# Kernel tuning notes

Hardware: AMD Instinct MI355X
Metric: run time of the kernel (lower is better)

The kernel has to match this reference:

```python
import jax, jax.numpy as jnp
import numpy as np

NUM_HEADS = 4
GROUPS = 8
EPS = 1e-5


def setup_inputs() -> dict:
    key = jax.random.key(0)
    ks = jax.random.split(key, 8)
    B, C, H, W = 8, 512, 64, 64
    L, E = 77, 768
    std = 0.02
    return {
        "x": jax.random.normal(ks[0], (B, C, H, W), jnp.float32),
        "text_emb": jax.random.normal(ks[1], (B, L, E), jnp.float32),
        "attention_mask": jax.random.randint(ks[2], (B, L), 0, 2, jnp.int32),
        "Wq_w": jax.random.normal(ks[3], (C, C), jnp.float32) * std,
        "Wq_b": jnp.zeros((C,), jnp.float32),
        "Wk_w": jax.random.normal(ks[4], (C, E), jnp.float32) * std,
        "Wk_b": jnp.zeros((C,), jnp.float32),
        "Wv_w": jax.random.normal(ks[5], (C, E), jnp.float32) * std,
        "Wv_b": jnp.zeros((C,), jnp.float32),
        "gn_scale": jnp.ones((C,), jnp.float32),
        "gn_bias": jnp.zeros((C,), jnp.float32),
    }


def reference(x, text_emb, attention_mask, Wq_w, Wq_b, Wk_w, Wk_b, Wv_w, Wv_b, gn_scale, gn_bias):
    B, C, H, W = x.shape
    dh = C // NUM_HEADS
    scale = dh ** -0.5

    # [B, HW, C] queries from image features
    x_flat = x.reshape(B, C, H * W).transpose(0, 2, 1)
    Q = x_flat @ Wq_w.T + Wq_b                 # [B, S, C]
    K = text_emb @ Wk_w.T + Wk_b               # [B, L, C]
    V = text_emb @ Wv_w.T + Wv_b               # [B, L, C]

    def split_heads(t):
        Bt, T, _ = t.shape
        return t.reshape(Bt, T, NUM_HEADS, dh).transpose(0, 2, 1, 3)  # [B, h, T, dh]

    Qh, Kh, Vh = split_heads(Q), split_heads(K), split_heads(V)

    scores = jnp.einsum("bhqd,bhkd->bhqk", Qh, Kh) * scale  # [B, h, S, L]
    mask = (attention_mask == 0)[:, None, None, :]
    scores = jnp.where(mask, -jnp.inf, scores)
    probs = jax.nn.softmax(scores, axis=-1)
    # dropout layers are identity in eval mode
    attn = jnp.einsum("bhqk,bhkd->bhqd", probs, Vh)          # [B, h, S, dh]

    out = attn.transpose(0, 2, 1, 3).reshape(B, H * W, C)    # [B, S, C]
    out = out.transpose(0, 2, 1).reshape(B, C, H, W)

    # GroupNorm(8 groups, affine) over (C/G, H, W) per group
    g = out.reshape(B, GROUPS, -1)
    mean = g.mean(axis=-1, keepdims=True)
    var = g.var(axis=-1, keepdims=True)
    g = (g - mean) * jax.lax.rsqrt(var + EPS)
    out = g.reshape(B, C, H, W) * gn_scale[None, :, None, None] + gn_bias[None, :, None, None]
    return out
```

## Files before the change

kernel.cpp:

```cpp
#include <hip/hip_runtime.h>
#include <hip/hip_bf16.h>
#include <cstdint>


typedef __attribute__((ext_vector_type(8))) short short8;
typedef __attribute__((ext_vector_type(4))) short short4v;
typedef __attribute__((ext_vector_type(4))) float f32x4;

#define DEV __device__ __forceinline__

DEV float bf2f(unsigned short u){ union{uint32_t i; float f;} x; x.i = ((uint32_t)u) << 16; return x.f; }
DEV unsigned short f2bf(float f){ __hip_bfloat16 h = __float2bfloat16(&f ? f : f); return *reinterpret_cast<unsigned short*>(&h); }
DEV short8 ld8(const unsigned short* p){ return *reinterpret_cast<const short8*>(p); }
DEV f32x4 ldf4(const float* p){ return *reinterpret_cast<const f32x4*>(p); }

#if defined(__has_builtin)
#if __has_builtin(__builtin_amdgcn_global_load_lds)
#define HAVE_ASYNC_LDS 1
#endif
#endif

__global__ __launch_bounds__(256) void k_fat(const float* __restrict__ x,
                                             unsigned short* __restrict__ xT,
                                             const float* __restrict__ text,
                                             const float* __restrict__ Wk,
                                             const float* __restrict__ Wkb,
                                             const float* __restrict__ Wv,
                                             const float* __restrict__ Wvb,
                                             unsigned short* __restrict__ wsK,
                                             unsigned short* __restrict__ wsVt,
                                             const float* __restrict__ Wq,
                                             unsigned short* __restrict__ wsWqT,
                                             int b0, int s_base, int slen, int SB){
  __shared__ unsigned short U[10368];
  const int tid = threadIdx.x;
  const int bx = blockIdx.x, by = blockIdx.y, bz = blockIdx.z;
  const int bg = b0 + bz;

  if (bx < 64){
    if (bx * 64 >= slen) return;
    unsigned short* t = U;
    const int s0 = s_base + bx * 64, c0 = by * 64;
    #pragma unroll
    for (int it = 0; it < 2; ++it){
      int slot = tid + it * 256;
      int r = slot >> 3, sg = slot & 7;
      int sw = sg ^ (r >> 3);
      const float* src = &x[((size_t)(bg * 512 + c0 + r)) * 4096 + s0 + sg * 8];
      f32x4 a = ldf4(src), b = ldf4(src + 4);
      short8 v;
      #pragma unroll
      for (int j = 0; j < 4; ++j){ v[j] = (short)f2bf(a[j]); v[j + 4] = (short)f2bf(b[j]); }
      *reinterpret_cast<short8*>(&t[r * 72 + sw * 8]) = v;
    }
    __syncthreads();
    #pragma unroll
    for (int it = 0; it < 2; ++it){
      int slot = tid + it * 256;
      int j = slot >> 3, i8 = slot & 7;
      short8 v;
      #pragma unroll
      for (int q = 0; q < 8; ++q){
        int c = i8 * 8 + q;
        int sw = (j >> 3) ^ i8;
        v[q] = (short)t[c * 72 + sw * 8 + (j & 7)];
      }
      *reinterpret_cast<short8*>(&xT[((size_t)(bz * slen) + bx * 64 + j) * 512 + c0 + i8 * 8]) = v;
    }
  } else if (bx < 66){
    unsigned short* At = U;
    unsigned short* Bt = U + 5760;
    const int wave = tid >> 6, lane = tid & 63;
    const int m16 = lane & 15, quad = lane >> 4;
    const int uc = (bx - 64) * 8 + by;
    const int u0 = uc * 64;
    const bool isK = (u0 < 512);
    const float* W  = isK ? Wk  : Wv;
    const float* Wb = isK ? Wkb : Wvb;
    const int c0 = u0 & 511;
    const int c  = c0 + wave * 16 + m16;
    f32x4 acc[5];
    #pragma unroll
    for (int mt = 0; mt < 5; ++mt) acc[mt] = (f32x4){0.f, 0.f, 0.f, 0.f};
    for (int kc = 0; kc < 12; ++kc){
      const int e0 = kc * 64;
      #pragma unroll
      for (int it = 0; it < 9; ++it){
        int slot = tid + it * 256;
        if (slot < 1280){
          int row = slot >> 4, e4 = (slot & 15) * 4;
          f32x4 v = (row < 77) ? ldf4(&text[((size_t)(bg * 77 + row)) * 768 + e0 + e4])
                               : (f32x4){0.f, 0.f, 0.f, 0.f};
          short4v o;
          #pragma unroll
          for (int j = 0; j < 4; ++j) o[j] = (short)f2bf(v[j]);
          *reinterpret_cast<short4v*>(&At[row * 72 + e4]) = o;
        } else {
          int bs = slot - 1280;
          int row = bs >> 4, e4 = (bs & 15) * 4;
          f32x4 v = ldf4(&W[((size_t)(c0 + row)) * 768 + e0 + e4]);
          short4v o;
          #pragma unroll
          for (int j = 0; j < 4; ++j) o[j] = (short)f2bf(v[j]);
          *reinterpret_cast<short4v*>(&Bt[row * 72 + e4]) = o;
        }
      }
      __syncthreads();
      #pragma unroll
      for (int kk = 0; kk < 64; kk += 32){
        short8 bf_ = *reinterpret_cast<const short8*>(&Bt[(wave * 16 + m16) * 72 + kk + quad * 8]);
        #pragma unroll
        for (int mt = 0; mt < 5; ++mt){
          short8 af_ = *reinterpret_cast<const short8*>(&At[(mt * 16 + m16) * 72 + kk + quad * 8]);
          acc[mt] = __builtin_amdgcn_mfma_f32_16x16x32_bf16(af_, bf_, acc[mt], 0, 0, 0);
        }
      }
      __syncthreads();
    }
    const float bias = Wb[c];
    if (isK){
      #pragma unroll
      for (int mt = 0; mt < 5; ++mt)
        #pragma unroll
        for (int r = 0; r < 4; ++r){
          int l = mt * 16 + quad * 4 + r;
          if (l < 77) wsK[((size_t)(bz * 77 + l)) * 512 + c] = f2bf(acc[mt][r] + bias);
        }
    } else {
      unsigned short* vr = &wsVt[((size_t)(bz * 512 + c)) * 96];
      #pragma unroll
      for (int mt = 0; mt < 5; ++mt){
        short4v pk;
        #pragma unroll
        for (int r = 0; r < 4; ++r) pk[r] = (short)f2bf(acc[mt][r] + bias);
        *reinterpret_cast<short4v*>(&vr[mt * 16 + quad * 4]) = pk;
      }
      short4v z = {};
      *reinterpret_cast<short4v*>(&vr[80 + quad * 4]) = z;
    }
  } else {
    unsigned short* t = U;
    const int nb = 8 * SB;
    const int p  = by + bz * 8;
    for (int tile = p; tile < 64; tile += nb){
      const int ti = tile >> 3, tj = tile & 7;
      #pragma unroll
      for (int it = 0; it < 2; ++it){
        int slot = tid + it * 256;
        int r = slot >> 3, sg = slot & 7;
        int sw = sg ^ (r >> 3);
        const float* src = &Wq[((size_t)(tj * 64 + r)) * 512 + ti * 64 + sg * 8];
        f32x4 a = ldf4(src), b2 = ldf4(src + 4);
        short8 v;
        #pragma unroll
        for (int j = 0; j < 4; ++j){ v[j] = (short)f2bf(a[j]); v[j + 4] = (short)f2bf(b2[j]); }
        *reinterpret_cast<short8*>(&t[r * 72 + sw * 8]) = v;
      }
      __syncthreads();
      #pragma unroll
      for (int it = 0; it < 2; ++it){
        int slot = tid + it * 256;
        int j = slot >> 3, i8 = slot & 7;
        short8 v;
        #pragma unroll
        for (int q = 0; q < 8; ++q){
          int dd = i8 * 8 + q;
          int sw = (j >> 3) ^ i8;
          v[q] = (short)t[dd * 72 + sw * 8 + (j & 7)];
        }
        *reinterpret_cast<short8*>(&wsWqT[((size_t)(ti * 64 + j)) * 512 + tj * 64 + i8 * 8]) = v;
      }
      __syncthreads();
    }
  }
}

__global__ __launch_bounds__(256) void k1b(const unsigned short* __restrict__ wsWqT,
                                           const unsigned short* __restrict__ wsK,
                                           const float* __restrict__ Wqb,
                                           unsigned short* __restrict__ wsKWq,
                                           float* __restrict__ kbias){
  const int tid = threadIdx.x;
  const int wave = tid >> 6, lane = tid & 63;
  const int m16 = lane & 15, quad = lane >> 4;
  const int cq = blockIdx.x, h = blockIdx.y, bz = blockIdx.z;
  const int cbase = cq * 128 + wave * 32;

  f32x4 acc[2][5];
  #pragma unroll
  for (int mt = 0; mt < 2; ++mt)
    #pragma unroll
    for (int nt = 0; nt < 5; ++nt) acc[mt][nt] = (f32x4){0.f, 0.f, 0.f, 0.f};

  #pragma unroll
  for (int ks = 0; ks < 4; ++ks){
    short8 aw[2];
    #pragma unroll
    for (int mt = 0; mt < 2; ++mt)
      aw[mt] = ld8(&wsWqT[(size_t)(cbase + mt * 16 + m16) * 512 + h * 128 + ks * 32 + quad * 8]);
    #pragma unroll
    for (int nt = 0; nt < 5; ++nt){
      int l = nt * 16 + m16;
      short8 bk = {};
      if (l < 77) bk = ld8(&wsK[((size_t)(bz * 77 + l)) * 512 + h * 128 + ks * 32 + quad * 8]);
      #pragma unroll
      for (int mt = 0; mt < 2; ++mt)
        acc[mt][nt] = __builtin_amdgcn_mfma_f32_16x16x32_bf16(aw[mt], bk, acc[mt][nt], 0, 0, 0);
    }
  }
  #pragma unroll
  for (int mt = 0; mt < 2; ++mt)
    #pragma unroll
    for (int nt = 0; nt < 5; ++nt){
      int l = nt * 16 + m16;
      short4v pk;
      #pragma unroll
      for (int r = 0; r < 4; ++r) pk[r] = (short)f2bf(acc[mt][nt][r]);
      *reinterpret_cast<short4v*>(&wsKWq[((size_t)((bz * 4 + h) * 80 + l)) * 512 + cbase + mt * 16 + quad * 4]) = pk;
    }
  if (cq == 0 && tid < 80){
    int l = tid;
    float kb = 0.f;
    if (l < 77){
      #pragma unroll
      for (int d = 0; d < 128; d += 8){
        short8 kv = ld8(&wsK[((size_t)(bz * 77 + l)) * 512 + h * 128 + d]);
        f32x4 wa = ldf4(&Wqb[h * 128 + d]);
        f32x4 wb = ldf4(&Wqb[h * 128 + d + 4]);
        #pragma unroll
        for (int j = 0; j < 4; ++j){
          kb += bf2f((unsigned short)kv[j]) * wa[j];
          kb += bf2f((unsigned short)kv[j + 4]) * wb[j];
        }
      }
    }
    kbias[(bz * 4 + h) * 80 + l] = kb;
  }
}

__global__ __launch_bounds__(256, 4) void k2_attn(const unsigned short* __restrict__ xT,
                                                  const unsigned short* __restrict__ wsKWq,
                                                  const unsigned short* __restrict__ wsVt,
                                                  const int* __restrict__ amask,
                                                  const float* __restrict__ kbias,
                                                  float* __restrict__ out,
                                                  float* __restrict__ gnacc,
                                                  int b0, int s_base, int slen){
  __shared__ unsigned short arena[13312];
  __shared__ float maskf[96];
  unsigned short* Pt = arena;

  const int tid = threadIdx.x;
  const int wave = tid >> 6, lane = tid & 63;
  const int m16 = lane & 15, quad = lane >> 4;
  const int st = blockIdx.x, h = blockIdx.y, bz = blockIdx.z;
  const int bg = b0 + bz;
  const int s_glob = s_base + st * 128;
  const int R0 = (wave >> 1) * 64, C0 = (wave & 1) * 64;
  const int sw0 = wave * 32;
  const float scale = 0.08838834764831845f;

  if (tid < 96){
    int l = tid;
    float mbv = -30000.f;
    if (l < 77 && amask[bg * 77 + l] != 0) mbv = kbias[(bz * 4 + h) * 80 + l] * scale;
    maskf[l] = mbv;
  }

  const unsigned short* Abase = wsKWq + (size_t)((bz * 4 + h) * 80) * 512;
  const unsigned short* Bbase = xT + ((size_t)bz * slen + st * 128 + sw0) * 512;

  f32x4 acc2[5][2];
  #pragma unroll
  for (int mt = 0; mt < 5; ++mt){ acc2[mt][0] = (f32x4){0.f,0.f,0.f,0.f}; acc2[mt][1] = (f32x4){0.f,0.f,0.f,0.f}; }

  auto stageA = [&](int kc, int buf){
    const int sbase = buf * 5120;
    #pragma unroll
    for (int it = 0; it < 3; ++it){
      const int ubase = it * 256 + wave * 64;
      if (ubase < 640){
        const int u = ubase + lane;
        int l = u >> 3, pos = (u & 7) ^ (l & 7);
        const unsigned short* src = Abase + (size_t)l * 512 + kc * 64 + pos * 8;
#ifdef HAVE_ASYNC_LDS
        __builtin_amdgcn_global_load_lds((const __attribute__((address_space(1))) void*)src,
                                         (__attribute__((address_space(3))) void*)&arena[sbase + ubase * 8],
                                         16, 0, 0);
#else
        *reinterpret_cast<short8*>(&arena[sbase + u * 8]) = ld8(src);
#endif
      }
    }
  };

  short8 Breg[2][4];
  auto loadB = [&](int kc, int buf){
    #pragma unroll
    for (int nt = 0; nt < 2; ++nt)
      #pragma unroll
      for (int kk = 0; kk < 2; ++kk)
        Breg[buf][nt * 2 + kk] = ld8(&Bbase[(size_t)(nt * 16 + m16) * 512 + kc * 64 + kk * 32 + quad * 8]);
  };

  auto compute = [&](int buf){
    const int ab = buf * 5120;
    #pragma unroll
    for (int kk = 0; kk < 2; ++kk){
      short8 af[5];
      #pragma unroll
      for (int mt = 0; mt < 5; ++mt){
        int l = mt * 16 + m16;
        int p = (kk * 4 + quad) ^ (l & 7);
        af[mt] = *reinterpret_cast<const short8*>(&arena[ab + l * 64 + p * 8]);
      }
      #pragma unroll
      for (int mt = 0; mt < 5; ++mt)
        #pragma unroll
        for (int nt = 0; nt < 2; ++nt)
          acc2[mt][nt] = __builtin_amdgcn_mfma_f32_16x16x32_bf16(af[mt], Breg[buf][nt * 2 + kk], acc2[mt][nt], 0, 0, 0);
    }
  };

  stageA(0, 0);
  loadB(0, 0);
  __syncthreads();
  #pragma unroll
  for (int kc = 0; kc < 8; ++kc){
    if (kc < 7){ stageA(kc + 1, (kc + 1) & 1); loadB(kc + 1, (kc + 1) & 1); }
    compute(kc & 1);
    __syncthreads();
  }

  const unsigned short* Vb = wsVt + (size_t)(bz * 512 + h * 128) * 96;
  short8 av0[4];
  #pragma unroll
  for (int mt = 0; mt < 4; ++mt)
    av0[mt] = ld8(&Vb[(size_t)(R0 + mt * 16 + m16) * 96 + quad * 8]);

  {
    float mb[5][4];
    #pragma unroll
    for (int mt = 0; mt < 5; ++mt)
      #pragma unroll
      for (int r = 0; r < 4; ++r) mb[mt][r] = maskf[mt * 16 + quad * 4 + r];
    #pragma unroll
    for (int nt = 0; nt < 2; ++nt){
      float sv[5][4]; float mx = -3e38f;
      #pragma unroll
      for (int mt = 0; mt < 5; ++mt)
        #pragma unroll
        for (int r = 0; r < 4; ++r){
          float v = acc2[mt][nt][r] * scale + mb[mt][r];
          sv[mt][r] = v; mx = fmaxf(mx, v);
        }
      mx = fmaxf(mx, __shfl_xor(mx, 16)); mx = fmaxf(mx, __shfl_xor(mx, 32));
      float sum = 0.f;
      #pragma unroll
      for (int mt = 0; mt < 5; ++mt)
        #pragma unroll
        for (int r = 0; r < 4; ++r){ float e = __expf(sv[mt][r] - mx); sv[mt][r] = e; sum += e; }
      sum += __shfl_xor(sum, 16); sum += __shfl_xor(sum, 32);
      float inv = 1.0f / sum;
      int sl = sw0 + nt * 16 + m16;
      #pragma unroll
      for (int mt = 0; mt < 5; ++mt){
        short4v pk;
        #pragma unroll
        for (int r = 0; r < 4; ++r) pk[r] = (short)f2bf(sv[mt][r] * inv);
        *reinterpret_cast<short4v*>(&Pt[sl * 104 + mt * 16 + quad * 4]) = pk;
      }
      short4v z = {};
      *reinterpret_cast<short4v*>(&Pt[sl * 104 + 80 + quad * 4]) = z;
    }
  }
  __syncthreads();

  f32x4 acc3[4][4];
  #pragma unroll
  for (int mt = 0; mt < 4; ++mt)
    #pragma unroll
    for (int nt = 0; nt < 4; ++nt) acc3[mt][nt] = (f32x4){0.f, 0.f, 0.f, 0.f};
  #pragma unroll
  for (int ks = 0; ks < 3; ++ks){
    short8 av[4], bp[4];
    #pragma unroll
    for (int mt = 0; mt < 4; ++mt)
      av[mt] = (ks == 0) ? av0[mt]
                         : ld8(&Vb[(size_t)(R0 + mt * 16 + m16) * 96 + ks * 32 + quad * 8]);
    #pragma unroll
    for (int nt = 0; nt < 4; ++nt)
      bp[nt] = *reinterpret_cast<const short8*>(&Pt[(C0 + nt * 16 + m16) * 104 + ks * 32 + quad * 8]);
    #pragma unroll
    for (int mt = 0; mt < 4; ++mt)
      #pragma unroll
      for (int nt = 0; nt < 4; ++nt)
        acc3[mt][nt] = __builtin_amdgcn_mfma_f32_16x16x32_bf16(av[mt], bp[nt], acc3[mt][nt], 0, 0, 0);
  }

  float sum = 0.f, ssq = 0.f;
  #pragma unroll
  for (int mt = 0; mt < 4; ++mt)
    #pragma unroll
    for (int nt = 0; nt < 4; ++nt)
      #pragma unroll
      for (int r = 0; r < 4; ++r){
        float v = acc3[mt][nt][r];
        sum += v; ssq += v * v;
      }
  #pragma unroll
  for (int off = 1; off < 64; off <<= 1){ sum += __shfl_xor(sum, off); ssq += __shfl_xor(ssq, off); }
  if (lane == 0){
    int g = h * 2 + (R0 >> 6);
    atomicAdd(&gnacc[(bg * 8 + g) * 2],     sum);
    atomicAdd(&gnacc[(bg * 8 + g) * 2 + 1], ssq);
  }

  __syncthreads();

  float* T = reinterpret_cast<float*>(arena);
  const int TS = 132;
  #pragma unroll
  for (int p = 0; p < 4; ++p){
    if ((R0 >> 6) == (p >> 1)){
      #pragma unroll
      for (int mt2 = 0; mt2 < 2; ++mt2){
        int mt = (p & 1) * 2 + mt2;
        #pragma unroll
        for (int nt = 0; nt < 4; ++nt)
          #pragma unroll
          for (int r = 0; r < 4; ++r)
            T[(mt2 * 16 + quad * 4 + r) * TS + C0 + nt * 16 + m16] = acc3[mt][nt][r];
      }
    }
    __syncthreads();
    #pragma unroll
    for (int it = 0; it < 4; ++it){
      int row = wave * 8 + it * 2 + (lane >> 5);
      int c = h * 128 + p * 32 + row;
      int sc = (lane & 31) * 4;
      f32x4 v = *reinterpret_cast<const f32x4*>(&T[row * TS + sc]);
      *reinterpret_cast<f32x4*>(&out[(size_t)(bg * 512 + c) * 4096 + s_glob + sc]) = v;
    }
    __syncthreads();
  }
}

__global__ __launch_bounds__(256) void k3_gn(float* __restrict__ out,
                                             const float* __restrict__ gnacc,
                                             const float* __restrict__ gns,
                                             const float* __restrict__ gnb){
  const int bx = blockIdx.x;
  const int b = bx >> 9, c = bx & 511;
  const int g = c >> 6;
  const float s  = gnacc[(b * 8 + g) * 2];
  const float ss = gnacc[(b * 8 + g) * 2 + 1];
  const float invN = 1.f / 262144.f;
  const float mean = s * invN;
  const float var  = ss * invN - mean * mean;
  const float rstd = rsqrtf(fmaxf(var, 0.f) + 1e-5f);
  const float a  = rstd * gns[c];
  const float bb = gnb[c] - mean * a;
  const size_t base = (size_t)bx * 4096;
  #pragma unroll
  for (int p = 0; p < 4; ++p){
    size_t off = base + p * 1024 + threadIdx.x * 4;
    f32x4 v = ldf4(&out[off]);
    f32x4 o;
    #pragma unroll
    for (int j = 0; j < 4; ++j) o[j] = v[j] * a + bb;
    *reinterpret_cast<f32x4*>(&out[off]) = o;
  }
}

extern "C" void kernel_launch(void* const* d_in, const int* in_sizes, int n_in,
                              void* d_out, int out_size, void* d_ws, size_t ws_size,
                              hipStream_t stream){
  (void)in_sizes; (void)n_in; (void)out_size;
  const float* x    = (const float*)d_in[0];
  const float* text = (const float*)d_in[1];
  const int*   am   = (const int*)d_in[2];
  const float* Wq   = (const float*)d_in[3];
  const float* Wqb  = (const float*)d_in[4];
  const float* Wk   = (const float*)d_in[5];
  const float* Wkb  = (const float*)d_in[6];
  const float* Wv   = (const float*)d_in[7];
  const float* Wvb  = (const float*)d_in[8];
  const float* gns  = (const float*)d_in[9];
  const float* gnb  = (const float*)d_in[10];
  float* out = (float*)d_out;

  auto need = [](int SB, int SLEN) -> size_t {
    return 512ull + 524288ull + (size_t)SB * 506112ull + (size_t)SB * SLEN * 1024ull;
  };
  int SB = 8, SLEN = 4096;
  if      (ws_size >= need(8, 4096)) { SB = 8; SLEN = 4096; }
  else if (ws_size >= need(4, 4096)) { SB = 4; SLEN = 4096; }
  else if (ws_size >= need(2, 4096)) { SB = 2; SLEN = 4096; }
  else if (ws_size >= need(1, 4096)) { SB = 1; SLEN = 4096; }
  else if (ws_size >= need(1, 1024)) { SB = 1; SLEN = 1024; }
  else                               { SB = 1; SLEN = 256;  }

  uint8_t* ws = (uint8_t*)d_ws;
  float*          gnacc = (float*)ws;
  unsigned short* wsWqT = (unsigned short*)(ws + 512);
  unsigned short* wsK   = wsWqT + 512 * 512;
  unsigned short* wsVt  = wsK  + (size_t)SB * 77 * 512;
  unsigned short* wsKWq = wsVt + (size_t)SB * 512 * 96;
  float*          kbias = (float*)(wsKWq + (size_t)SB * 4 * 80 * 512);
  unsigned short* xT    = (unsigned short*)(kbias + (size_t)SB * 4 * 80);

  hipMemsetAsync(gnacc, 0, 128 * sizeof(float), stream);
  for (int b0 = 0; b0 < 8; b0 += SB){
    for (int s_base = 0; s_base < 4096; s_base += SLEN){
      k_fat<<<dim3(67, 8, SB), 256, 0, stream>>>(x, xT, text, Wk, Wkb, Wv, Wvb,
                                                 wsK, wsVt, Wq, wsWqT, b0, s_base, SLEN, SB);
      if (s_base == 0)
        k1b<<<dim3(4, 4, SB), 256, 0, stream>>>(wsWqT, wsK, Wqb, wsKWq, kbias);
      k2_attn<<<dim3(SLEN / 128, 4, SB), 256, 0, stream>>>(xT, wsKWq, wsVt, am, kbias,
                                                           out, gnacc, b0, s_base, SLEN);
    }
  }
  k3_gn<<<4096, 256, 0, stream>>>(out, gnacc, gns, gnb);
}
```

Before: 140.4 us.

## Fuse GroupNorm into attention kernel via grid-wide atomic barrier

The attention kernel now waits at a grid-wide barrier (atomic counter plus spin) until every block has added its GroupNorm partial sums. It then computes mean and rstd and applies the affine normalization directly while storing the output. This removes the separate GroupNorm pass, which re-read and re-wrote the whole output tensor. The cost is that correctness depends on all 1024 blocks being co-resident; otherwise the spin will deadlock. Blocks also sit idle at the barrier, and the smaller-workspace fallback keeps the old path.

```diff
diff --git a/kernel.cpp b/kernel.cpp
--- a/kernel.cpp
+++ b/kernel.cpp
@@ -10,7 +10,7 @@
 #define DEV __device__ __forceinline__
 
 DEV float bf2f(unsigned short u){ union{uint32_t i; float f;} x; x.i = ((uint32_t)u) << 16; return x.f; }
-DEV unsigned short f2bf(float f){ __hip_bfloat16 h = __float2bfloat16(&f ? f : f); return *reinterpret_cast<unsigned short*>(&h); }
+DEV unsigned short f2bf(float f){ __hip_bfloat16 h = __float2bfloat16(f); return *reinterpret_cast<unsigned short*>(&h); }
 DEV short8 ld8(const unsigned short* p){ return *reinterpret_cast<const short8*>(p); }
 DEV f32x4 ldf4(const float* p){ return *reinterpret_cast<const f32x4*>(p); }
 
@@ -245,7 +245,10 @@
                                                   const float* __restrict__ kbias,
                                                   float* __restrict__ out,
                                                   float* __restrict__ gnacc,
-                                                  int b0, int s_base, int slen){
+                                                  int* __restrict__ sync_cnt,
+                                                  const float* __restrict__ gns,
+                                                  const float* __restrict__ gnb,
+                                                  int b0, int s_base, int slen, int doGN){
   __shared__ unsigned short arena[13312];
   __shared__ float maskf[96];
   unsigned short* Pt = arena;
@@ -418,6 +421,24 @@
 
   __syncthreads();
 
+  float mean0 = 0.f, rstd0 = 1.f, mean1 = 0.f, rstd1 = 1.f;
+  if (doGN){
+    const int nblocks = gridDim.x * gridDim.y * gridDim.z;
+    if (tid == 0){
+      __hip_atomic_fetch_add(sync_cnt, 1, __ATOMIC_RELEASE, __HIP_MEMORY_SCOPE_AGENT);
+      while (__hip_atomic_load(sync_cnt, __ATOMIC_ACQUIRE, __HIP_MEMORY_SCOPE_AGENT) < nblocks)
+        __builtin_amdgcn_s_sleep(8);
+    }
+    __syncthreads();
+    const float invN = 1.f / 262144.f;
+    float sv0 = __hip_atomic_load(&gnacc[(bg * 8 + h * 2) * 2],     __ATOMIC_RELAXED, __HIP_MEMORY_SCOPE_AGENT);
+    float sq0 = __hip_atomic_load(&gnacc[(bg * 8 + h * 2) * 2 + 1], __ATOMIC_RELAXED, __HIP_MEMORY_SCOPE_AGENT);
+    float sv1 = __hip_atomic_load(&gnacc[(bg * 8 + h * 2 + 1) * 2],     __ATOMIC_RELAXED, __HIP_MEMORY_SCOPE_AGENT);
+    float sq1 = __hip_atomic_load(&gnacc[(bg * 8 + h * 2 + 1) * 2 + 1], __ATOMIC_RELAXED, __HIP_MEMORY_SCOPE_AGENT);
+    mean0 = sv0 * invN; rstd0 = rsqrtf(fmaxf(sq0 * invN - mean0 * mean0, 0.f) + 1e-5f);
+    mean1 = sv1 * invN; rstd1 = rsqrtf(fmaxf(sq1 * invN - mean1 * mean1, 0.f) + 1e-5f);
+  }
+
   float* T = reinterpret_cast<float*>(arena);
   const int TS = 132;
   #pragma unroll
@@ -434,13 +455,24 @@
       }
     }
     __syncthreads();
+    const float mean = (p >> 1) ? mean1 : mean0;
+    const float rstd = (p >> 1) ? rstd1 : rstd0;
     #pragma unroll
     for (int it = 0; it < 4; ++it){
       int row = wave * 8 + it * 2 + (lane >> 5);
       int c = h * 128 + p * 32 + row;
       int sc = (lane & 31) * 4;
       f32x4 v = *reinterpret_cast<const f32x4*>(&T[row * TS + sc]);
-      *reinterpret_cast<f32x4*>(&out[(size_t)(bg * 512 + c) * 4096 + s_glob + sc]) = v;
+      f32x4 o;
+      if (doGN){
+        float aa = rstd * gns[c];
+        float bb = gnb[c] - mean * aa;
+        #pragma unroll
+        for (int j = 0; j < 4; ++j) o[j] = v[j] * aa + bb;
+      } else {
+        o = v;
+      }
+      *reinterpret_cast<f32x4*>(&out[(size_t)(bg * 512 + c) * 4096 + s_glob + sc]) = o;
     }
     __syncthreads();
   }
@@ -491,7 +523,7 @@
   float* out = (float*)d_out;
 
   auto need = [](int SB, int SLEN) -> size_t {
-    return 512ull + 524288ull + (size_t)SB * 506112ull + (size_t)SB * SLEN * 1024ull;
+    return 1024ull + 524288ull + (size_t)SB * 506112ull + (size_t)SB * SLEN * 1024ull;
   };
   int SB = 8, SLEN = 4096;
   if      (ws_size >= need(8, 4096)) { SB = 8; SLEN = 4096; }
@@ -503,23 +535,30 @@
 
   uint8_t* ws = (uint8_t*)d_ws;
   float*          gnacc = (float*)ws;
-  unsigned short* wsWqT = (unsigned short*)(ws + 512);
+  int*            scnt  = (int*)(ws + 512);
+  unsigned short* wsWqT = (unsigned short*)(ws + 1024);
   unsigned short* wsK   = wsWqT + 512 * 512;
   unsigned short* wsVt  = wsK  + (size_t)SB * 77 * 512;
   unsigned short* wsKWq = wsVt + (size_t)SB * 512 * 96;
   float*          kbias = (float*)(wsKWq + (size_t)SB * 4 * 80 * 512);
   unsigned short* xT    = (unsigned short*)(kbias + (size_t)SB * 4 * 80);
 
-  hipMemsetAsync(gnacc, 0, 128 * sizeof(float), stream);
+  const int doGN = (SLEN == 4096) ? 1 : 0;
+
+  hipMemsetAsync(ws, 0, 1024, stream);
   for (int b0 = 0; b0 < 8; b0 += SB){
     for (int s_base = 0; s_base < 4096; s_base += SLEN){
       k_fat<<<dim3(67, 8, SB), 256, 0, stream>>>(x, xT, text, Wk, Wkb, Wv, Wvb,
                                                  wsK, wsVt, Wq, wsWqT, b0, s_base, SLEN, SB);
       if (s_base == 0)
         k1b<<<dim3(4, 4, SB), 256, 0, stream>>>(wsWqT, wsK, Wqb, wsKWq, kbias);
+      if (doGN)
+        hipMemsetAsync(scnt, 0, sizeof(int), stream);
       k2_attn<<<dim3(SLEN / 128, 4, SB), 256, 0, stream>>>(xT, wsKWq, wsVt, am, kbias,
-                                                           out, gnacc, b0, s_base, SLEN);
-    }
-  }
-  k3_gn<<<4096, 256, 0, stream>>>(out, gnacc, gns, gnb);
+                                                           out, gnacc, scnt, gns, gnb,
+                                                           b0, s_base, SLEN, doGN);
+    }
+  }
+  if (!doGN)
+    k3_gn<<<4096, 256, 0, stream>>>(out, gnacc, gns, gnb);
 }
```

After: 232.8 us. +65.8%, slower.
